# Optimization experiments

Hardware: AMD Instinct MI355X
Metric: run time of the kernel (lower is better)

The kernel has to match this reference:

```python
import jax, jax.numpy as jnp
import numpy as np

B, S, D = 4, 2048, 512
H, DQK, DV = 6, 64, 64
PROJ = (DQK + DQK + DV) * H  # 1152
EPS = 1e-5


def setup_inputs() -> dict:
    key = jax.random.key(0)
    ks = jax.random.split(key, 5)
    sc = 0.05
    return {
        "x": jax.random.normal(ks[0], (B, S, D), jnp.float32),
        "Wp": jax.random.normal(ks[1], (PROJ, D), jnp.float32) * sc,
        "bp": jax.random.normal(ks[2], (PROJ,), jnp.float32) * sc,
        "Wo": jax.random.normal(ks[3], (D, H * DV), jnp.float32) * sc,
        "bo": jax.random.normal(ks[4], (D,), jnp.float32) * sc,
        "gamma": jnp.ones((D,), jnp.float32),
        "beta": jnp.zeros((D,), jnp.float32),
    }


def reference(x, Wp, bp, Wo, bo, gamma, beta):
    b, s, d = x.shape
    # 1x1 Conv1d projection == pointwise linear: [b,s,d] @ [d,proj] -> [b,s,proj]
    proj = jnp.einsum("bsd,pd->bsp", x, Wp) + bp
    q, k, v = proj[..., : H * DQK], proj[..., H * DQK : 2 * H * DQK], proj[..., 2 * H * DQK :]
    # split heads -> [b,h,s,depth]
    q = q.reshape(b, s, H, DQK).transpose(0, 2, 1, 3)
    k = k.reshape(b, s, H, DQK).transpose(0, 2, 1, 3)
    v = v.reshape(b, s, H, DV).transpose(0, 2, 1, 3)
    scores = jnp.einsum("bhqd,bhkd->bhqk", q, k) / jnp.sqrt(jnp.float32(DQK))
    attn = jax.nn.softmax(scores, axis=-1)  # softmax over kv axis
    out = jnp.einsum("bhqk,bhkd->bhqd", attn, v)
    # concat heads -> [b,s,h*dv]
    concat = out.transpose(0, 2, 1, 3).reshape(b, s, H * DV)
    y = jnp.einsum("bsf,df->bsd", concat, Wo) + bo
    z = x + y
    mu = jnp.mean(z, axis=-1, keepdims=True)
    var = jnp.mean(jnp.square(z - mu), axis=-1, keepdims=True)
    return (z - mu) / jnp.sqrt(var + EPS) * gamma + beta
```

## Files before the change

### kernel.cpp

```cpp
#include <hip/hip_runtime.h>

typedef __bf16 bf16;
typedef __bf16 bf16x8 __attribute__((ext_vector_type(8)));
typedef __bf16 bf16x4 __attribute__((ext_vector_type(4)));
typedef float  f32x4  __attribute__((ext_vector_type(4)));

#define BB 4
#define SS 2048
#define DD 512
#define HH 6
#define DH 64
#define PROJ 1152
#define FF 384
#define LDK 72

__device__ __forceinline__ bool probe_fp32(const unsigned* p) {
    return p[0] == 0x3F800000u;
}

__device__ __forceinline__ void async16(const bf16* g, bf16* l) {
    __builtin_amdgcn_global_load_lds(
        (const __attribute__((address_space(1))) void*)g,
        (__attribute__((address_space(3))) void*)l, 16, 0, 0);
}

struct CvtSrcs { const void* s[7]; };

#define CB0 524288
#define CB1 598016
#define CB2 622592
#define CB3 622736
#define CB4 622800
#define CB5 622864
#define CB6 622928

__global__ __launch_bounds__(256) void cvt_all_kernel(
    CvtSrcs srcs, bf16* __restrict__ dst, const unsigned* __restrict__ probe)
{
    const int t = blockIdx.x * 256 + threadIdx.x;
    if (t >= CB6) return;
    int seg, base;
    if      (t < CB0) { seg = 0; base = 0;   }
    else if (t < CB1) { seg = 1; base = CB0; }
    else if (t < CB2) { seg = 2; base = CB1; }
    else if (t < CB3) { seg = 3; base = CB2; }
    else if (t < CB4) { seg = 4; base = CB3; }
    else if (t < CB5) { seg = 5; base = CB4; }
    else              { seg = 6; base = CB5; }
    const int li = (t - base) * 8;
    if (probe_fp32(probe)) {
        const float* s = (const float*)srcs.s[seg] + li;
        bf16x8 o;
#pragma unroll
        for (int j = 0; j < 8; ++j) o[j] = (bf16)s[j];
        *(bf16x8*)&dst[(size_t)t * 8] = o;
    } else {
        *(bf16x8*)&dst[(size_t)t * 8] =
            *(const bf16x8*)((const bf16*)srcs.s[seg] + li);
    }
}

__global__ __launch_bounds__(256) void gemm_bt_kernel(
    const bf16* __restrict__ A, const bf16* __restrict__ B,
    const bf16* __restrict__ bias, void* __restrict__ Cout,
    int M, int N, int K, int store_f32)
{
    __shared__ __attribute__((aligned(16))) bf16 sA[8192];
    __shared__ __attribute__((aligned(16))) bf16 sB[8192];

    const int tid  = threadIdx.x;
    const int lane = tid & 63;
    const int wave = tid >> 6;
    const int wmb = (wave >> 1) * 4;
    const int wnb = (wave & 1) * 4;
    const int l15 = lane & 15;
    const int quad = lane >> 4;
    const int bm = blockIdx.x * 128;
    const int bn = blockIdx.y * 128;

    const bf16* pA[4];
    const bf16* pB[4];
#pragma unroll
    for (int j = 0; j < 4; ++j) {
        int c = wave * 4 + j;
        int row = (c >> 1) * 16 + (lane & 15);
        int col = ((c & 1) << 5) + (lane >> 4) * 8;
        pA[j] = A + (size_t)(bm + row) * K + col;
        pB[j] = B + (size_t)(bn + row) * K + col;
    }

    const f32x4 fzero = {0.f, 0.f, 0.f, 0.f};
    f32x4 acc[4][4];
#pragma unroll
    for (int mi = 0; mi < 4; ++mi)
#pragma unroll
        for (int ni = 0; ni < 4; ++ni) acc[mi][ni] = fzero;

    for (int k0 = 0; k0 < K; k0 += 64) {
        __syncthreads();
#pragma unroll
        for (int j = 0; j < 4; ++j) {
            int c = wave * 4 + j;
            async16(pA[j], &sA[c * 512]);
            async16(pB[j], &sB[c * 512]);
            pA[j] += 64;
            pB[j] += 64;
        }
        __syncthreads();

#pragma unroll
        for (int kk = 0; kk < 2; ++kk) {
            bf16x8 af[4], bfr[4];
#pragma unroll
            for (int i = 0; i < 4; ++i) {
                af[i]  = *(const bf16x8*)&sA[((wmb + i) * 128 + kk * 64 + quad * 16 + l15) * 8];
                bfr[i] = *(const bf16x8*)&sB[((wnb + i) * 128 + kk * 64 + quad * 16 + l15) * 8];
            }
#pragma unroll
            for (int mi = 0; mi < 4; ++mi)
#pragma unroll
                for (int ni = 0; ni < 4; ++ni)
                    acc[mi][ni] = __builtin_amdgcn_mfma_f32_16x16x32_bf16(
                        af[mi], bfr[ni], acc[mi][ni], 0, 0, 0);
        }
    }

#pragma unroll
    for (int mi = 0; mi < 4; ++mi) {
        int row = bm + (wmb + mi) * 16 + quad * 4;
#pragma unroll
        for (int ni = 0; ni < 4; ++ni) {
            int col = bn + (wnb + ni) * 16 + l15;
            float bv = (float)bias[col];
#pragma unroll
            for (int r = 0; r < 4; ++r) {
                float v = acc[mi][ni][r] + bv;
                if (store_f32) ((float*)Cout)[(size_t)(row + r) * N + col] = v;
                else           ((bf16*)Cout)[(size_t)(row + r) * N + col] = (bf16)v;
            }
        }
    }
}

__global__ __launch_bounds__(256) void vt_kernel(
    const bf16* __restrict__ proj, bf16* __restrict__ Vt)
{
    __shared__ __attribute__((aligned(16))) bf16 lt[64 * LDK];

    const int tid = threadIdx.x;
    const int s0 = blockIdx.x * 64;
    const int bh = blockIdx.y;
    const int b = bh / HH, h = bh % HH;

#pragma unroll
    for (int i = 0; i < 2; ++i) {
        int vid = i * 256 + tid;
        int sl = vid >> 3;
        int dc = (vid & 7) << 3;
        bf16x8 v = *(const bf16x8*)&proj[
            (size_t)(b * SS + s0 + sl) * PROJ + 2 * HH * DH + h * DH + dc];
#pragma unroll
        for (int j = 0; j < 8; ++j) {
            int d = dc + j;
            lt[d * LDK + (sl ^ (((d >> 3) & 3) * 8))] = v[j];
        }
    }
    __syncthreads();

#pragma unroll
    for (int i = 0; i < 2; ++i) {
        int vid = i * 256 + tid;
        int d = vid >> 3;
        int sc = (vid & 7) << 3;
        bf16x8 v = *(const bf16x8*)&lt[d * LDK + (sc ^ (((d >> 3) & 3) * 8))];
        *(bf16x8*)&Vt[(size_t)bh * DH * SS + (size_t)d * SS + s0 + sc] = v;
    }
}

__global__ __launch_bounds__(256) void attn_kernel(
    const bf16* __restrict__ proj, const bf16* __restrict__ Vt,
    bf16* __restrict__ concat)
{
    __shared__ __attribute__((aligned(16))) bf16 sK [64 * LDK];
    __shared__ __attribute__((aligned(16))) bf16 sVt[64 * LDK];
    __shared__ __attribute__((aligned(16))) bf16 sP [4 * 16 * LDK];

    const int tid  = threadIdx.x;
    const int lane = tid & 63;
    const int wave = tid >> 6;
    const int l15  = lane & 15;
    const int quad = lane >> 4;

    const int bh = blockIdx.y;
    const int b = bh / HH, h = bh % HH;
    const int q0 = blockIdx.x * 64;
    const bf16* base = proj + (size_t)b * SS * PROJ;
    const bf16* vtb  = Vt + (size_t)bh * DH * SS;

    const int sr = tid >> 3;
    const int sc = (tid & 7) << 3;

    const int qrow = q0 + wave * 16 + l15;
    bf16x8 qf[2];
    qf[0] = *(const bf16x8*)&base[(size_t)qrow * PROJ + h * DH + quad * 8];
    qf[1] = *(const bf16x8*)&base[(size_t)qrow * PROJ + h * DH + 32 + quad * 8];
#pragma unroll
    for (int j = 0; j < 8; ++j) {
        qf[0][j] = (bf16)((float)qf[0][j] * 0.125f);
        qf[1][j] = (bf16)((float)qf[1][j] * 0.125f);
    }

    const f32x4 fzero = {0.f, 0.f, 0.f, 0.f};
    float l_part = 0.f;
    f32x4 oacc[4];
#pragma unroll
    for (int fi = 0; fi < 4; ++fi) oacc[fi] = fzero;

    bf16* pw = &sP[wave * 16 * LDK];

    bf16x8 kreg[2], vreg[2];
#pragma unroll
    for (int i = 0; i < 2; ++i) {
        int r = i * 32 + sr;
        kreg[i] = *(const bf16x8*)&base[(size_t)r * PROJ + HH * DH + h * DH + sc];
        vreg[i] = *(const bf16x8*)&vtb[(size_t)r * SS + sc];
    }

    for (int kt = 0; kt < SS / 64; ++kt) {
        __syncthreads();
#pragma unroll
        for (int i = 0; i < 2; ++i) {
            int r = i * 32 + sr;
            *(bf16x8*)&sK [r * LDK + sc] = kreg[i];
            *(bf16x8*)&sVt[r * LDK + sc] = vreg[i];
        }
        __syncthreads();
        if (kt + 1 < SS / 64) {
#pragma unroll
            for (int i = 0; i < 2; ++i) {
                int r = i * 32 + sr;
                kreg[i] = *(const bf16x8*)&base[
                    (size_t)((kt + 1) * 64 + r) * PROJ + HH * DH + h * DH + sc];
                vreg[i] = *(const bf16x8*)&vtb[(size_t)r * SS + (kt + 1) * 64 + sc];
            }
        }

        f32x4 st[4];
#pragma unroll
        for (int mi = 0; mi < 4; ++mi) st[mi] = fzero;
#pragma unroll
        for (int ks = 0; ks < 2; ++ks)
#pragma unroll
            for (int mi = 0; mi < 4; ++mi) {
                bf16x8 af = *(const bf16x8*)&sK[(mi * 16 + l15) * LDK + ks * 32 + quad * 8];
                st[mi] = __builtin_amdgcn_mfma_f32_16x16x32_bf16(af, qf[ks], st[mi], 0, 0, 0);
            }

#pragma unroll
        for (int mi = 0; mi < 4; ++mi)
#pragma unroll
            for (int r = 0; r < 4; ++r) {
                st[mi][r] = __expf(st[mi][r]);
                l_part += st[mi][r];
            }

#pragma unroll
        for (int mi = 0; mi < 4; ++mi) {
            bf16x4 p4;
#pragma unroll
            for (int r = 0; r < 4; ++r) p4[r] = (bf16)st[mi][r];
            *(bf16x4*)&pw[l15 * LDK + mi * 16 + quad * 4] = p4;
        }

#pragma unroll
        for (int ks = 0; ks < 2; ++ks) {
            bf16x8 bfrag = *(const bf16x8*)&pw[l15 * LDK + ks * 32 + quad * 8];
#pragma unroll
            for (int fi = 0; fi < 4; ++fi) {
                bf16x8 af = *(const bf16x8*)&sVt[(fi * 16 + l15) * LDK + ks * 32 + quad * 8];
                oacc[fi] = __builtin_amdgcn_mfma_f32_16x16x32_bf16(af, bfrag, oacc[fi], 0, 0, 0);
            }
        }
    }

    float l = l_part;
    l += __shfl_xor(l, 16);
    l += __shfl_xor(l, 32);
    float invl = 1.f / l;

    const int qg = q0 + wave * 16 + l15;
    bf16* crow = concat + (size_t)(b * SS + qg) * FF + h * DH;
#pragma unroll
    for (int fi = 0; fi < 4; ++fi) {
        bf16x4 o4;
#pragma unroll
        for (int r = 0; r < 4; ++r) o4[r] = (bf16)(oacc[fi][r] * invl);
        *(bf16x4*)&crow[fi * 16 + quad * 4] = o4;
    }
}

__global__ __launch_bounds__(256) void ln_kernel(
    const void* __restrict__ xr, const float* __restrict__ y,
    const bf16* __restrict__ gamma, const bf16* __restrict__ beta,
    void* __restrict__ out, const unsigned* __restrict__ probe)
{
    const bool f32 = probe_fp32(probe);
    const int lane = threadIdx.x & 63;
    const int wave = threadIdx.x >> 6;
    const int row = blockIdx.x * 4 + wave;
    const size_t off = (size_t)row * DD + lane * 8;

    float z[8];
    if (f32) {
        const float* xf = (const float*)xr;
#pragma unroll
        for (int j = 0; j < 8; ++j) z[j] = xf[off + j];
    } else {
        bf16x8 xv = *(const bf16x8*)&((const bf16*)xr)[off];
#pragma unroll
        for (int j = 0; j < 8; ++j) z[j] = (float)xv[j];
    }
    f32x4 y0 = *(const f32x4*)&y[off];
    f32x4 y1 = *(const f32x4*)&y[off + 4];
#pragma unroll
    for (int j = 0; j < 4; ++j) { z[j] += y0[j]; z[j + 4] += y1[j]; }

    float s = 0.f;
#pragma unroll
    for (int j = 0; j < 8; ++j) s += z[j];
#pragma unroll
    for (int m = 1; m < 64; m <<= 1) s += __shfl_xor(s, m);
    float mu = s * (1.f / DD);
    float s2 = 0.f;
#pragma unroll
    for (int j = 0; j < 8; ++j) { float d = z[j] - mu; s2 += d * d; }
#pragma unroll
    for (int m = 1; m < 64; m <<= 1) s2 += __shfl_xor(s2, m);
    float rs = rsqrtf(s2 * (1.f / DD) + 1e-5f);

    bf16x8 g  = *(const bf16x8*)&gamma[lane * 8];
    bf16x8 be = *(const bf16x8*)&beta[lane * 8];
    if (f32) {
        f32x4 o0, o1;
#pragma unroll
        for (int j = 0; j < 4; ++j) {
            o0[j] = (z[j]     - mu) * rs * (float)g[j]     + (float)be[j];
            o1[j] = (z[j + 4] - mu) * rs * (float)g[j + 4] + (float)be[j + 4];
        }
        *(f32x4*)&((float*)out)[off]     = o0;
        *(f32x4*)&((float*)out)[off + 4] = o1;
    } else {
        bf16x8 o;
#pragma unroll
        for (int j = 0; j < 8; ++j)
            o[j] = (bf16)((z[j] - mu) * rs * (float)g[j] + (float)be[j]);
        *(bf16x8*)&((bf16*)out)[off] = o;
    }
}

extern "C" void kernel_launch(void* const* d_in, const int* in_sizes, int n_in,
                              void* d_out, int out_size, void* d_ws, size_t ws_size,
                              hipStream_t stream)
{
    const unsigned* probe = (const unsigned*)d_in[5];

    char* ws = (char*)d_ws;
    size_t o = 0;
    bf16* xb   = (bf16*)(ws + o); o += (size_t)BB * SS * DD * 2;
    bf16* Wpb  = (bf16*)(ws + o); o += (size_t)PROJ * DD * 2;
    bf16* Wob  = (bf16*)(ws + o); o += (size_t)DD * FF * 2;
    bf16* bpb  = (bf16*)(ws + o); o += PROJ * 2;
    bf16* bob  = (bf16*)(ws + o); o += DD * 2;
    bf16* gb   = (bf16*)(ws + o); o += DD * 2;
    bf16* bb   = (bf16*)(ws + o); o += DD * 2;
    bf16* proj = (bf16*)(ws + o); o += (size_t)BB * SS * PROJ * 2;
    bf16* concat = (bf16*)(ws + o); o += (size_t)BB * SS * FF * 2;
    bf16* vtbuf  = (bf16*)(ws + o); o += (size_t)BB * HH * DH * SS * 2;
    float* ybuf = (float*)proj;

    CvtSrcs srcs;
    srcs.s[0] = d_in[0]; srcs.s[1] = d_in[1]; srcs.s[2] = d_in[3];
    srcs.s[3] = d_in[2]; srcs.s[4] = d_in[4]; srcs.s[5] = d_in[5];
    srcs.s[6] = d_in[6];
    cvt_all_kernel<<<(CB6 + 255) / 256, 256, 0, stream>>>(srcs, xb, probe);

    gemm_bt_kernel<<<dim3((BB * SS) / 128, PROJ / 128), 256, 0, stream>>>(
        xb, Wpb, bpb, proj, BB * SS, PROJ, DD, 0);
    vt_kernel<<<dim3(SS / 64, BB * HH), 256, 0, stream>>>(proj, vtbuf);
    attn_kernel<<<dim3(SS / 64, BB * HH), 256, 0, stream>>>(proj, vtbuf, concat);
    gemm_bt_kernel<<<dim3((BB * SS) / 128, DD / 128), 256, 0, stream>>>(
        concat, Wob, bob, ybuf, BB * SS, DD, FF, 1);
    ln_kernel<<<dim3((BB * SS) / 4), 256, 0, stream>>>(
        d_in[0], ybuf, gb, bb, d_out, probe);
}
```

Measured before the change: 193.8 us.

## Split attention KV range across two blocks and double query tile per wave

The attention kernel now has each wave process 32 query rows instead of 16, so every K/V fragment loaded from LDS feeds twice as many MFMAs. The KV sequence is also split into two halves across blockIdx.z, keeping the grid at 768 blocks. Each half writes unnormalized partial outputs and row sums, and a new merge kernel sums the two halves and normalizes into concat. The trade is an extra launch plus partial-buffer traffic, and more registers per wave, in exchange for better reuse of K/V loads. The softmax has no max subtraction, so the partial sums combine by simple addition.

```diff
diff --git a/kernel.cpp b/kernel.cpp
--- a/kernel.cpp
+++ b/kernel.cpp
@@ -179,11 +179,11 @@
 
 __global__ __launch_bounds__(256) void attn_kernel(
     const bf16* __restrict__ proj, const bf16* __restrict__ Vt,
-    bf16* __restrict__ concat)
+    bf16* __restrict__ Opart, float* __restrict__ lpart)
 {
     __shared__ __attribute__((aligned(16))) bf16 sK [64 * LDK];
     __shared__ __attribute__((aligned(16))) bf16 sVt[64 * LDK];
-    __shared__ __attribute__((aligned(16))) bf16 sP [4 * 16 * LDK];
+    __shared__ __attribute__((aligned(16))) bf16 sP [4 * 32 * LDK];
 
     const int tid  = threadIdx.x;
     const int lane = tid & 63;
@@ -193,40 +193,50 @@
 
     const int bh = blockIdx.y;
     const int b = bh / HH, h = bh % HH;
-    const int q0 = blockIdx.x * 64;
+    const int q0 = blockIdx.x * 128;
+    const int kz = blockIdx.z;
     const bf16* base = proj + (size_t)b * SS * PROJ;
     const bf16* vtb  = Vt + (size_t)bh * DH * SS;
 
     const int sr = tid >> 3;
     const int sc = (tid & 7) << 3;
 
-    const int qrow = q0 + wave * 16 + l15;
-    bf16x8 qf[2];
-    qf[0] = *(const bf16x8*)&base[(size_t)qrow * PROJ + h * DH + quad * 8];
-    qf[1] = *(const bf16x8*)&base[(size_t)qrow * PROJ + h * DH + 32 + quad * 8];
-#pragma unroll
-    for (int j = 0; j < 8; ++j) {
-        qf[0][j] = (bf16)((float)qf[0][j] * 0.125f);
-        qf[1][j] = (bf16)((float)qf[1][j] * 0.125f);
+    bf16x8 qf[2][2];
+#pragma unroll
+    for (int g = 0; g < 2; ++g) {
+        const int qrow = q0 + wave * 32 + g * 16 + l15;
+#pragma unroll
+        for (int ks = 0; ks < 2; ++ks) {
+            qf[ks][g] = *(const bf16x8*)&base[
+                (size_t)qrow * PROJ + h * DH + ks * 32 + quad * 8];
+#pragma unroll
+            for (int j = 0; j < 8; ++j)
+                qf[ks][g][j] = (bf16)((float)qf[ks][g][j] * 0.125f);
+        }
     }
 
     const f32x4 fzero = {0.f, 0.f, 0.f, 0.f};
-    float l_part = 0.f;
-    f32x4 oacc[4];
-#pragma unroll
-    for (int fi = 0; fi < 4; ++fi) oacc[fi] = fzero;
-
-    bf16* pw = &sP[wave * 16 * LDK];
+    float l_part[2] = {0.f, 0.f};
+    f32x4 oacc[2][4];
+#pragma unroll
+    for (int g = 0; g < 2; ++g)
+#pragma unroll
+        for (int fi = 0; fi < 4; ++fi) oacc[g][fi] = fzero;
+
+    bf16* pw = &sP[wave * 32 * LDK];
+
+    const int kt0 = kz * (SS / 128);
+    const int kt1 = kt0 + SS / 128;
 
     bf16x8 kreg[2], vreg[2];
 #pragma unroll
     for (int i = 0; i < 2; ++i) {
         int r = i * 32 + sr;
-        kreg[i] = *(const bf16x8*)&base[(size_t)r * PROJ + HH * DH + h * DH + sc];
-        vreg[i] = *(const bf16x8*)&vtb[(size_t)r * SS + sc];
-    }
-
-    for (int kt = 0; kt < SS / 64; ++kt) {
+        kreg[i] = *(const bf16x8*)&base[(size_t)(kt0 * 64 + r) * PROJ + HH * DH + h * DH + sc];
+        vreg[i] = *(const bf16x8*)&vtb[(size_t)r * SS + kt0 * 64 + sc];
+    }
+
+    for (int kt = kt0; kt < kt1; ++kt) {
         __syncthreads();
 #pragma unroll
         for (int i = 0; i < 2; ++i) {
@@ -235,7 +245,7 @@
             *(bf16x8*)&sVt[r * LDK + sc] = vreg[i];
         }
         __syncthreads();
-        if (kt + 1 < SS / 64) {
+        if (kt + 1 < kt1) {
 #pragma unroll
             for (int i = 0; i < 2; ++i) {
                 int r = i * 32 + sr;
@@ -245,58 +255,106 @@
             }
         }
 
-        f32x4 st[4];
-#pragma unroll
-        for (int mi = 0; mi < 4; ++mi) st[mi] = fzero;
+        f32x4 st[2][4];
+#pragma unroll
+        for (int g = 0; g < 2; ++g)
+#pragma unroll
+            for (int mi = 0; mi < 4; ++mi) st[g][mi] = fzero;
 #pragma unroll
         for (int ks = 0; ks < 2; ++ks)
 #pragma unroll
             for (int mi = 0; mi < 4; ++mi) {
                 bf16x8 af = *(const bf16x8*)&sK[(mi * 16 + l15) * LDK + ks * 32 + quad * 8];
-                st[mi] = __builtin_amdgcn_mfma_f32_16x16x32_bf16(af, qf[ks], st[mi], 0, 0, 0);
-            }
-
-#pragma unroll
-        for (int mi = 0; mi < 4; ++mi)
-#pragma unroll
-            for (int r = 0; r < 4; ++r) {
-                st[mi][r] = __expf(st[mi][r]);
-                l_part += st[mi][r];
-            }
-
-#pragma unroll
-        for (int mi = 0; mi < 4; ++mi) {
-            bf16x4 p4;
-#pragma unroll
-            for (int r = 0; r < 4; ++r) p4[r] = (bf16)st[mi][r];
-            *(bf16x4*)&pw[l15 * LDK + mi * 16 + quad * 4] = p4;
-        }
+#pragma unroll
+                for (int g = 0; g < 2; ++g)
+                    st[g][mi] = __builtin_amdgcn_mfma_f32_16x16x32_bf16(
+                        af, qf[ks][g], st[g][mi], 0, 0, 0);
+            }
+
+#pragma unroll
+        for (int g = 0; g < 2; ++g)
+#pragma unroll
+            for (int mi = 0; mi < 4; ++mi)
+#pragma unroll
+                for (int r = 0; r < 4; ++r) {
+                    st[g][mi][r] = __expf(st[g][mi][r]);
+                    l_part[g] += st[g][mi][r];
+                }
+
+#pragma unroll
+        for (int g = 0; g < 2; ++g)
+#pragma unroll
+            for (int mi = 0; mi < 4; ++mi) {
+                bf16x4 p4;
+#pragma unroll
+                for (int r = 0; r < 4; ++r) p4[r] = (bf16)st[g][mi][r];
+                *(bf16x4*)&pw[(g * 16 + l15) * LDK + mi * 16 + quad * 4] = p4;
+            }
 
 #pragma unroll
         for (int ks = 0; ks < 2; ++ks) {
-            bf16x8 bfrag = *(const bf16x8*)&pw[l15 * LDK + ks * 32 + quad * 8];
+            bf16x8 bfrag[2];
+#pragma unroll
+            for (int g = 0; g < 2; ++g)
+                bfrag[g] = *(const bf16x8*)&pw[(g * 16 + l15) * LDK + ks * 32 + quad * 8];
 #pragma unroll
             for (int fi = 0; fi < 4; ++fi) {
                 bf16x8 af = *(const bf16x8*)&sVt[(fi * 16 + l15) * LDK + ks * 32 + quad * 8];
-                oacc[fi] = __builtin_amdgcn_mfma_f32_16x16x32_bf16(af, bfrag, oacc[fi], 0, 0, 0);
-            }
-        }
-    }
-
-    float l = l_part;
-    l += __shfl_xor(l, 16);
-    l += __shfl_xor(l, 32);
-    float invl = 1.f / l;
-
-    const int qg = q0 + wave * 16 + l15;
-    bf16* crow = concat + (size_t)(b * SS + qg) * FF + h * DH;
-#pragma unroll
-    for (int fi = 0; fi < 4; ++fi) {
-        bf16x4 o4;
-#pragma unroll
-        for (int r = 0; r < 4; ++r) o4[r] = (bf16)(oacc[fi][r] * invl);
-        *(bf16x4*)&crow[fi * 16 + quad * 4] = o4;
-    }
+#pragma unroll
+                for (int g = 0; g < 2; ++g)
+                    oacc[g][fi] = __builtin_amdgcn_mfma_f32_16x16x32_bf16(
+                        af, bfrag[g], oacc[g][fi], 0, 0, 0);
+            }
+        }
+    }
+
+#pragma unroll
+    for (int g = 0; g < 2; ++g) {
+        l_part[g] += __shfl_xor(l_part[g], 16);
+        l_part[g] += __shfl_xor(l_part[g], 32);
+    }
+
+    const size_t zoff = (size_t)(kz * BB * HH + bh) * SS;
+#pragma unroll
+    for (int g = 0; g < 2; ++g) {
+        const int qg = q0 + wave * 32 + g * 16 + l15;
+        bf16* orow = Opart + (zoff + qg) * DH;
+#pragma unroll
+        for (int fi = 0; fi < 4; ++fi) {
+            bf16x4 o4;
+#pragma unroll
+            for (int r = 0; r < 4; ++r) o4[r] = (bf16)oacc[g][fi][r];
+            *(bf16x4*)&orow[fi * 16 + quad * 4] = o4;
+        }
+    }
+    if (lane < 16) {
+#pragma unroll
+        for (int g = 0; g < 2; ++g)
+            lpart[zoff + q0 + wave * 32 + g * 16 + lane] = l_part[g];
+    }
+}
+
+__global__ __launch_bounds__(256) void attn_merge_kernel(
+    const bf16* __restrict__ Opart, const float* __restrict__ lpart,
+    bf16* __restrict__ concat)
+{
+    const int g = blockIdx.x * 256 + threadIdx.x;
+    const int d8 = g & 7;
+    const int q  = (g >> 3) & (SS - 1);
+    const int bh = g >> 14;
+    const int b = bh / HH, h = bh % HH;
+
+    const size_t off0 = ((size_t)bh * SS + q) * DH + d8 * 8;
+    const size_t off1 = ((size_t)(BB * HH + bh) * SS + q) * DH + d8 * 8;
+    bf16x8 a0 = *(const bf16x8*)&Opart[off0];
+    bf16x8 a1 = *(const bf16x8*)&Opart[off1];
+    float invl = 1.f / (lpart[(size_t)bh * SS + q] +
+                        lpart[(size_t)(BB * HH + bh) * SS + q]);
+    bf16x8 o;
+#pragma unroll
+    for (int j = 0; j < 8; ++j)
+        o[j] = (bf16)(((float)a0[j] + (float)a1[j]) * invl);
+    *(bf16x8*)&concat[((size_t)(b * SS + q)) * FF + h * DH + d8 * 8] = o;
 }
 
 __global__ __launch_bounds__(256) void ln_kernel(
@@ -338,14 +396,14 @@
     for (int m = 1; m < 64; m <<= 1) s2 += __shfl_xor(s2, m);
     float rs = rsqrtf(s2 * (1.f / DD) + 1e-5f);
 
-    bf16x8 g  = *(const bf16x8*)&gamma[lane * 8];
+    bf16x8 gm = *(const bf16x8*)&gamma[lane * 8];
     bf16x8 be = *(const bf16x8*)&beta[lane * 8];
     if (f32) {
         f32x4 o0, o1;
 #pragma unroll
         for (int j = 0; j < 4; ++j) {
-            o0[j] = (z[j]     - mu) * rs * (float)g[j]     + (float)be[j];
-            o1[j] = (z[j + 4] - mu) * rs * (float)g[j + 4] + (float)be[j + 4];
+            o0[j] = (z[j]     - mu) * rs * (float)gm[j]     + (float)be[j];
+            o1[j] = (z[j + 4] - mu) * rs * (float)gm[j + 4] + (float)be[j + 4];
         }
         *(f32x4*)&((float*)out)[off]     = o0;
         *(f32x4*)&((float*)out)[off + 4] = o1;
@@ -353,7 +411,7 @@
         bf16x8 o;
 #pragma unroll
         for (int j = 0; j < 8; ++j)
-            o[j] = (bf16)((z[j] - mu) * rs * (float)g[j] + (float)be[j]);
+            o[j] = (bf16)((z[j] - mu) * rs * (float)gm[j] + (float)be[j]);
         *(bf16x8*)&((bf16*)out)[off] = o;
     }
 }
@@ -376,6 +434,8 @@
     bf16* proj = (bf16*)(ws + o); o += (size_t)BB * SS * PROJ * 2;
     bf16* concat = (bf16*)(ws + o); o += (size_t)BB * SS * FF * 2;
     bf16* vtbuf  = (bf16*)(ws + o); o += (size_t)BB * HH * DH * SS * 2;
+    bf16* Opart  = (bf16*)(ws + o); o += (size_t)2 * BB * HH * SS * DH * 2;
+    float* lpart = (float*)(ws + o); o += (size_t)2 * BB * HH * SS * 4;
     float* ybuf = (float*)proj;
 
     CvtSrcs srcs;
@@ -387,7 +447,10 @@
     gemm_bt_kernel<<<dim3((BB * SS) / 128, PROJ / 128), 256, 0, stream>>>(
         xb, Wpb, bpb, proj, BB * SS, PROJ, DD, 0);
     vt_kernel<<<dim3(SS / 64, BB * HH), 256, 0, stream>>>(proj, vtbuf);
-    attn_kernel<<<dim3(SS / 64, BB * HH), 256, 0, stream>>>(proj, vtbuf, concat);
+    attn_kernel<<<dim3(SS / 128, BB * HH, 2), 256, 0, stream>>>(
+        proj, vtbuf, Opart, lpart);
+    attn_merge_kernel<<<(BB * HH * SS * 8) / 256, 256, 0, stream>>>(
+        Opart, lpart, concat);
     gemm_bt_kernel<<<dim3((BB * SS) / 128, DD / 128), 256, 0, stream>>>(
         concat, Wob, bob, ybuf, BB * SS, DD, FF, 1);
     ln_kernel<<<dim3((BB * SS) / 4), 256, 0, stream>>>(
```

Result: faster. 189.6 us (-2.2%).
